# Performance work log

Measured on AMD Instinct MI355X. Metric: run time of the kernel, lower is better.

The kernel has to match this reference:

```python
import jax, jax.numpy as jnp
import numpy as np

GROUP_SIZE = 64

def setup_inputs() -> dict:
    key = jax.random.key(0)
    ks = jax.random.split(key, 7)
    T, N, K, NG = 4096, 4096, 11264, 4096 // GROUP_SIZE
    x = jax.random.normal(ks[0], (T, N), dtype=jnp.float32)
    Q = jax.random.randint(ks[1], (K, N), 0, 8, dtype=jnp.int32)  # uint8 3-bit codes
    scales = jax.random.uniform(ks[2], (K, NG), dtype=jnp.float32)
    zeros = jax.random.uniform(ks[3], (K, NG), dtype=jnp.float32) * 7.0
    mu1 = jax.random.uniform(ks[4], (N,), dtype=jnp.float32) + 0.5
    mu2 = jax.random.uniform(ks[5], (K,), dtype=jnp.float32) + 0.5
    bias = jax.random.normal(ks[6], (K,), dtype=jnp.float32)
    return {"x": x, "Q": Q, "scales": scales, "zeros": zeros, "mu1": mu1, "mu2": mu2, "bias": bias}

def reference(x, Q, scales, zeros, mu1, mu2, bias):
    K, N = Q.shape
    ng = scales.shape[1]
    # group-wise dequant: (Q - zero) * scale, groups along N
    Qg = Q.astype(jnp.float32).reshape(K, ng, GROUP_SIZE)
    W_deq_norm = ((Qg - zeros[:, :, None]) * scales[:, :, None]).reshape(K, N)
    # Sinkhorn mu rescale: per-row mu2, per-column mu1
    W_deq = W_deq_norm * mu2[:, None] * mu1[None, :]
    out = x @ W_deq.T + bias
    return out
```

## Files before the change

kernel.cpp:

```cpp
#include <hip/hip_runtime.h>
#include <stdint.h>
#include <stddef.h>


typedef __attribute__((ext_vector_type(8))) short bfrag;
typedef __attribute__((ext_vector_type(4))) float f32x4;
typedef __attribute__((ext_vector_type(4))) int   i32x4;

__device__ __forceinline__ short f2bf(float f) {
    uint32_t u = __float_as_uint(f);
    u += 0x7fffu + ((u >> 16) & 1u);
    return (short)(u >> 16);
}

__device__ __forceinline__ void gload_lds16(const void* g, void* l) {
    __builtin_amdgcn_global_load_lds(
        (const __attribute__((address_space(1))) void*)g,
        (__attribute__((address_space(3))) void*)l,
        16, 0, 0);
}

__global__ void cvt_x_kernel(const float* __restrict__ x, short* __restrict__ xb) {
    size_t i = (size_t)blockIdx.x * 256 + threadIdx.x;
    const f32x4* xv = (const f32x4*)x + 4 * i;
    f32x4 a = xv[0], b = xv[1], c = xv[2], d = xv[3];
    bfrag o0, o1;
    o0[0] = f2bf(a[0]); o0[1] = f2bf(a[1]); o0[2] = f2bf(a[2]); o0[3] = f2bf(a[3]);
    o0[4] = f2bf(b[0]); o0[5] = f2bf(b[1]); o0[6] = f2bf(b[2]); o0[7] = f2bf(b[3]);
    o1[0] = f2bf(c[0]); o1[1] = f2bf(c[1]); o1[2] = f2bf(c[2]); o1[3] = f2bf(c[3]);
    o1[4] = f2bf(d[0]); o1[5] = f2bf(d[1]); o1[6] = f2bf(d[2]); o1[7] = f2bf(d[3]);
    bfrag* ov = (bfrag*)xb + 2 * i;
    ov[0] = o0; ov[1] = o1;
}

__global__ void deq_w_kernel(const int* __restrict__ Q,
                             const float* __restrict__ scales,
                             const float* __restrict__ zeros,
                             const float* __restrict__ mu1,
                             const float* __restrict__ mu2,
                             short* __restrict__ wb,
                             int k0, int N, int NG) {
    const int kl = blockIdx.x;
    const int kg = k0 + kl;
    const int t  = threadIdx.x;
    const int n0 = t << 4;
    const int g  = n0 >> 6;
    const float s = scales[(size_t)kg * NG + g] * mu2[kg];
    const float z = zeros[(size_t)kg * NG + g];
    const i32x4* qv = (const i32x4*)(Q + (size_t)kg * N + n0);
    const f32x4* uv = (const f32x4*)(mu1 + n0);
    i32x4 q0 = qv[0], q1 = qv[1], q2 = qv[2], q3 = qv[3];
    f32x4 u0 = uv[0], u1 = uv[1], u2 = uv[2], u3 = uv[3];
    bfrag o0, o1;
    o0[0] = f2bf(((float)q0[0] - z) * s * u0[0]);
    o0[1] = f2bf(((float)q0[1] - z) * s * u0[1]);
    o0[2] = f2bf(((float)q0[2] - z) * s * u0[2]);
    o0[3] = f2bf(((float)q0[3] - z) * s * u0[3]);
    o0[4] = f2bf(((float)q1[0] - z) * s * u1[0]);
    o0[5] = f2bf(((float)q1[1] - z) * s * u1[1]);
    o0[6] = f2bf(((float)q1[2] - z) * s * u1[2]);
    o0[7] = f2bf(((float)q1[3] - z) * s * u1[3]);
    o1[0] = f2bf(((float)q2[0] - z) * s * u2[0]);
    o1[1] = f2bf(((float)q2[1] - z) * s * u2[1]);
    o1[2] = f2bf(((float)q2[2] - z) * s * u2[2]);
    o1[3] = f2bf(((float)q2[3] - z) * s * u2[3]);
    o1[4] = f2bf(((float)q3[0] - z) * s * u3[0]);
    o1[5] = f2bf(((float)q3[1] - z) * s * u3[1]);
    o1[6] = f2bf(((float)q3[2] - z) * s * u3[2]);
    o1[7] = f2bf(((float)q3[3] - z) * s * u3[3]);
    bfrag* ov = (bfrag*)(wb + (size_t)kl * N + n0);
    ov[0] = o0; ov[1] = o1;
}


__global__ __launch_bounds__(512, 2)
void gemm8p_kernel(const short* __restrict__ A, const short* __restrict__ B,
                   const float* __restrict__ bias, float* __restrict__ C,
                   int Kc, int Nout, int col0, int GX) {
    extern __shared__ __attribute__((aligned(16))) char smem[];

    const int tid  = threadIdx.x;
    const int lane = tid & 63;
    const int wid  = tid >> 6;
    const int wm   = wid >> 2;
    const int wn   = wid & 3;
    const int r    = lane & 15;
    const int hib  = (lane >> 4) << 4;
    const int sw   = (r & 7) << 4;

    const int nwg = (int)gridDim.x;
    const int cpx = nwg >> 3;
    const int bid = (int)blockIdx.x;
    const int swz = (bid & 7) * cpx + (bid >> 3);
    const int bx  = swz % GX;
    const int by  = swz / GX;
    const int bm  = by * 256;
    const int bnl = bx * 256;

    const int KB = Kc * 2;
    const int swcol = ((tid ^ (tid >> 3)) & 7) << 4;
    const char* srcA = (const char*)A + (size_t)(bm  + (tid >> 3)) * KB + swcol;
    const char* srcB = (const char*)B + (size_t)(bnl + (tid >> 3)) * KB + swcol;

    f32x4 acc[8][4];
#pragma unroll
    for (int i = 0; i < 8; i++)
#pragma unroll
        for (int j = 0; j < 4; j++)
            acc[i][j] = (f32x4){0.f, 0.f, 0.f, 0.f};

    const int NT = Kc / 64;

#define STG_A(t, q) gload_lds16(srcA + (size_t)(t) * 128 + (size_t)(q) * 64 * KB, \
                                smem + ((t) & 1) * 65536 + (q) * 8192 + (tid << 4))
#define STG_B(t, q) gload_lds16(srcB + (size_t)(t) * 128 + (size_t)(q) * 64 * KB, \
                                smem + ((t) & 1) * 65536 + 32768 + (q) * 8192 + (tid << 4))
#define LDF(base, row, s) (*(const bfrag*)((base) + (size_t)(row) * 128 + (((s) * 64 + hib) ^ sw)))
#define MM(I, J, AF, BF) acc[I][J] = __builtin_amdgcn_mfma_f32_16x16x32_bf16(AF, BF, acc[I][J], 0, 0, 0)

#define PH(BUF, MQ, NQ, STAGES, VM) do {                                        \
    const char* Ab_ = smem + (BUF) * 65536;                                     \
    const char* Bb_ = Ab_ + 32768;                                              \
    const int ra_ = wm * 128 + (MQ) * 64 + r;                                   \
    const int rb_ = wn * 64 + (NQ) * 32 + r;                                    \
    bfrag a00_ = LDF(Ab_, ra_,      0), a01_ = LDF(Ab_, ra_,      1);           \
    bfrag a10_ = LDF(Ab_, ra_ + 16, 0), a11_ = LDF(Ab_, ra_ + 16, 1);           \
    bfrag a20_ = LDF(Ab_, ra_ + 32, 0), a21_ = LDF(Ab_, ra_ + 32, 1);           \
    bfrag a30_ = LDF(Ab_, ra_ + 48, 0), a31_ = LDF(Ab_, ra_ + 48, 1);           \
    bfrag b00_ = LDF(Bb_, rb_,      0), b01_ = LDF(Bb_, rb_,      1);           \
    bfrag b10_ = LDF(Bb_, rb_ + 16, 0), b11_ = LDF(Bb_, rb_ + 16, 1);           \
    STAGES;                                                                     \
    __builtin_amdgcn_s_barrier();                                               \
    asm volatile("s_waitcnt lgkmcnt(0)" ::: "memory");                          \
    __builtin_amdgcn_s_setprio(1);                                              \
    MM((MQ)*4 + 0, (NQ)*2 + 0, a00_, b00_); MM((MQ)*4 + 0, (NQ)*2 + 0, a01_, b01_); \
    MM((MQ)*4 + 0, (NQ)*2 + 1, a00_, b10_); MM((MQ)*4 + 0, (NQ)*2 + 1, a01_, b11_); \
    MM((MQ)*4 + 1, (NQ)*2 + 0, a10_, b00_); MM((MQ)*4 + 1, (NQ)*2 + 0, a11_, b01_); \
    MM((MQ)*4 + 1, (NQ)*2 + 1, a10_, b10_); MM((MQ)*4 + 1, (NQ)*2 + 1, a11_, b11_); \
    MM((MQ)*4 + 2, (NQ)*2 + 0, a20_, b00_); MM((MQ)*4 + 2, (NQ)*2 + 0, a21_, b01_); \
    MM((MQ)*4 + 2, (NQ)*2 + 1, a20_, b10_); MM((MQ)*4 + 2, (NQ)*2 + 1, a21_, b11_); \
    MM((MQ)*4 + 3, (NQ)*2 + 0, a30_, b00_); MM((MQ)*4 + 3, (NQ)*2 + 0, a31_, b01_); \
    MM((MQ)*4 + 3, (NQ)*2 + 1, a30_, b10_); MM((MQ)*4 + 3, (NQ)*2 + 1, a31_, b11_); \
    __builtin_amdgcn_s_setprio(0);                                              \
    VM;                                                                         \
    __builtin_amdgcn_s_barrier();                                               \
} while (0)

    STG_A(0, 0); STG_A(0, 1); STG_A(0, 2); STG_A(0, 3);
    STG_B(0, 0); STG_B(0, 1); STG_B(0, 2); STG_B(0, 3);
    STG_A(1, 0); STG_A(1, 2);
    asm volatile("s_waitcnt vmcnt(2)" ::: "memory");
    __builtin_amdgcn_s_barrier();

    for (int it = 0; it < NT / 2; ++it) {
        const int tb = 2 * it + 1;
        int tc = 2 * it + 2; if (tc > NT - 1) tc = NT - 1;
        int td = 2 * it + 3; if (td > NT - 1) td = NT - 1;
        PH(0, 0, 0, { STG_A(tb, 1); STG_A(tb, 3); STG_B(tb, 0); }, (void)0);
        PH(0, 0, 1, { STG_B(tb, 1); STG_B(tb, 2); STG_B(tb, 3); }, (void)0);
        PH(0, 1, 0, { STG_A(tc, 0); STG_A(tc, 2); }, (void)0);
        PH(0, 1, 1, {}, asm volatile("s_waitcnt vmcnt(2)" ::: "memory"));
        PH(1, 0, 0, { STG_A(tc, 1); STG_A(tc, 3); STG_B(tc, 0); }, (void)0);
        PH(1, 0, 1, { STG_B(tc, 1); STG_B(tc, 2); STG_B(tc, 3); }, (void)0);
        PH(1, 1, 0, { STG_A(td, 0); STG_A(td, 2); }, (void)0);
        PH(1, 1, 1, {}, asm volatile("s_waitcnt vmcnt(2)" ::: "memory"));
    }

#undef PH
#undef MM
#undef LDF
#undef STG_A
#undef STG_B

    const int row0 = bm + wm * 128 + (lane >> 4) * 4;
    const int colg = col0 + bnl + wn * 64 + r;
#pragma unroll
    for (int j = 0; j < 4; ++j) {
        const int col = colg + j * 16;
        const float bv = bias[col];
#pragma unroll
        for (int i = 0; i < 8; ++i) {
            const int row = row0 + i * 16;
#pragma unroll
            for (int q = 0; q < 4; ++q)
                C[(size_t)(row + q) * Nout + col] = acc[i][j][q] + bv;
        }
    }
}

__global__ void naive_kernel(const float* __restrict__ x, const int* __restrict__ Q,
                             const float* __restrict__ scales, const float* __restrict__ zeros,
                             const float* __restrict__ mu1, const float* __restrict__ mu2,
                             const float* __restrict__ bias, float* __restrict__ out,
                             int T, int N, int K, int NG) {
    long long total = (long long)T * K;
    for (long long idx = blockIdx.x * 256ll + threadIdx.x; idx < total;
         idx += (long long)gridDim.x * 256ll) {
        int t = (int)(idx / K);
        int k = (int)(idx - (long long)t * K);
        float s = 0.f;
        for (int n = 0; n < N; n++) {
            int g = n >> 6;
            float w = ((float)Q[(size_t)k * N + n] - zeros[(size_t)k * NG + g]) *
                      scales[(size_t)k * NG + g];
            s += x[(size_t)t * N + n] * w * mu1[n];
        }
        out[idx] = s * mu2[k] + bias[k];
    }
}

extern "C" void kernel_launch(void* const* d_in, const int* in_sizes, int n_in,
                              void* d_out, int out_size, void* d_ws, size_t ws_size,
                              hipStream_t stream) {
    const float* x      = (const float*)d_in[0];
    const int*   Q      = (const int*)d_in[1];
    const float* scales = (const float*)d_in[2];
    const float* zeros  = (const float*)d_in[3];
    const float* mu1    = (const float*)d_in[4];
    const float* mu2    = (const float*)d_in[5];
    const float* bias   = (const float*)d_in[6];
    float* out = (float*)d_out;

    const int N  = in_sizes[4];
    const int K  = in_sizes[5];
    const int T  = in_sizes[0] / N;
    const int NG = in_sizes[2] / K;

    const size_t xb_bytes  = (size_t)T * N * 2;
    const size_t row_bytes = (size_t)N * 2;

    const bool shape_ok = (T % 256 == 0) && (K % 256 == 0) &&
                          (N % 128 == 0) && (N % 64 == 0);

    if (!shape_ok || ws_size < xb_bytes + 256 * row_bytes) {
        naive_kernel<<<4096, 256, 0, stream>>>(x, Q, scales, zeros, mu1, mu2,
                                               bias, out, T, N, K, NG);
        return;
    }

    static bool attr_done = false;
    if (!attr_done) {
        (void)hipFuncSetAttribute(reinterpret_cast<const void*>(gemm8p_kernel),
                                  hipFuncAttributeMaxDynamicSharedMemorySize,
                                  131072);
        attr_done = true;
    }

    short* xb = (short*)d_ws;
    short* wb = (short*)((char*)d_ws + xb_bytes);
    size_t max_rows = (ws_size - xb_bytes) / row_bytes;
    int CH = (int)((max_rows / 256) * 256);
    if (CH > K) CH = K;

    cvt_x_kernel<<<(T * N / 16) / 256, 256, 0, stream>>>(x, xb);

    for (int c0 = 0; c0 < K; c0 += CH) {
        int rows = (K - c0 < CH) ? (K - c0) : CH;
        deq_w_kernel<<<rows, 256, 0, stream>>>(Q, scales, zeros, mu1, mu2, wb,
                                               c0, N, NG);
        const int GX = rows / 256;
        dim3 ggrid(GX * (T / 256));
        gemm8p_kernel<<<ggrid, 512, 131072, stream>>>(xb, wb, bias, out,
                                                      N, K, c0, GX);
    }
}
```

Measured before the change: 732.5 us.

## Reuse LDS fragments across GEMM quadrants and use grid-stride prep kernels

The GEMM main loop now keeps the A and B fragments in register arrays and reorders the quadrant visits as 00, 01, 11, 10, so A or B fragments are reused across consecutive quadrants. This cuts LDS reads per K-step (A read twice instead of four times, B read twice per buffer) at the cost of holding more fragment registers live. The x conversion and weight dequant kernels become grid-stride/row-loop kernels that handle 4 elements per thread per step, and the shape check now requires N divisible by 1024. The extra live fragments may raise register pressure at 2 waves per SIMD occupancy.

Result: faster. 684.9 us (-6.5%).

```diff
diff --git a/kernel.cpp b/kernel.cpp
--- a/kernel.cpp
+++ b/kernel.cpp
@@ -4,6 +4,7 @@
 
 
 typedef __attribute__((ext_vector_type(8))) short bfrag;
+typedef __attribute__((ext_vector_type(4))) short s16x4;
 typedef __attribute__((ext_vector_type(4))) float f32x4;
 typedef __attribute__((ext_vector_type(4))) int   i32x4;
 
@@ -20,17 +21,16 @@
         16, 0, 0);
 }
 
-__global__ void cvt_x_kernel(const float* __restrict__ x, short* __restrict__ xb) {
-    size_t i = (size_t)blockIdx.x * 256 + threadIdx.x;
-    const f32x4* xv = (const f32x4*)x + 4 * i;
-    f32x4 a = xv[0], b = xv[1], c = xv[2], d = xv[3];
-    bfrag o0, o1;
-    o0[0] = f2bf(a[0]); o0[1] = f2bf(a[1]); o0[2] = f2bf(a[2]); o0[3] = f2bf(a[3]);
-    o0[4] = f2bf(b[0]); o0[5] = f2bf(b[1]); o0[6] = f2bf(b[2]); o0[7] = f2bf(b[3]);
-    o1[0] = f2bf(c[0]); o1[1] = f2bf(c[1]); o1[2] = f2bf(c[2]); o1[3] = f2bf(c[3]);
-    o1[4] = f2bf(d[0]); o1[5] = f2bf(d[1]); o1[6] = f2bf(d[2]); o1[7] = f2bf(d[3]);
-    bfrag* ov = (bfrag*)xb + 2 * i;
-    ov[0] = o0; ov[1] = o1;
+__global__ void cvt_x_kernel(const float* __restrict__ x, short* __restrict__ xb,
+                             int total4) {
+    for (int i = blockIdx.x * 256 + threadIdx.x; i < total4;
+         i += gridDim.x * 256) {
+        f32x4 a = ((const f32x4*)x)[i];
+        s16x4 o;
+        o[0] = f2bf(a[0]); o[1] = f2bf(a[1]);
+        o[2] = f2bf(a[2]); o[3] = f2bf(a[3]);
+        ((s16x4*)xb)[i] = o;
+    }
 }
 
 __global__ void deq_w_kernel(const int* __restrict__ Q,
@@ -42,34 +42,24 @@
                              int k0, int N, int NG) {
     const int kl = blockIdx.x;
     const int kg = k0 + kl;
-    const int t  = threadIdx.x;
-    const int n0 = t << 4;
-    const int g  = n0 >> 6;
-    const float s = scales[(size_t)kg * NG + g] * mu2[kg];
-    const float z = zeros[(size_t)kg * NG + g];
-    const i32x4* qv = (const i32x4*)(Q + (size_t)kg * N + n0);
-    const f32x4* uv = (const f32x4*)(mu1 + n0);
-    i32x4 q0 = qv[0], q1 = qv[1], q2 = qv[2], q3 = qv[3];
-    f32x4 u0 = uv[0], u1 = uv[1], u2 = uv[2], u3 = uv[3];
-    bfrag o0, o1;
-    o0[0] = f2bf(((float)q0[0] - z) * s * u0[0]);
-    o0[1] = f2bf(((float)q0[1] - z) * s * u0[1]);
-    o0[2] = f2bf(((float)q0[2] - z) * s * u0[2]);
-    o0[3] = f2bf(((float)q0[3] - z) * s * u0[3]);
-    o0[4] = f2bf(((float)q1[0] - z) * s * u1[0]);
-    o0[5] = f2bf(((float)q1[1] - z) * s * u1[1]);
-    o0[6] = f2bf(((float)q1[2] - z) * s * u1[2]);
-    o0[7] = f2bf(((float)q1[3] - z) * s * u1[3]);
-    o1[0] = f2bf(((float)q2[0] - z) * s * u2[0]);
-    o1[1] = f2bf(((float)q2[1] - z) * s * u2[1]);
-    o1[2] = f2bf(((float)q2[2] - z) * s * u2[2]);
-    o1[3] = f2bf(((float)q2[3] - z) * s * u2[3]);
-    o1[4] = f2bf(((float)q3[0] - z) * s * u3[0]);
-    o1[5] = f2bf(((float)q3[1] - z) * s * u3[1]);
-    o1[6] = f2bf(((float)q3[2] - z) * s * u3[2]);
-    o1[7] = f2bf(((float)q3[3] - z) * s * u3[3]);
-    bfrag* ov = (bfrag*)(wb + (size_t)kl * N + n0);
-    ov[0] = o0; ov[1] = o1;
+    const float m2 = mu2[kg];
+    const int*   qrow = Q + (size_t)kg * N;
+    const float* srow = scales + (size_t)kg * NG;
+    const float* zrow = zeros + (size_t)kg * NG;
+    short*       orow = wb + (size_t)kl * N;
+    for (int n0 = threadIdx.x * 4; n0 < N; n0 += 1024) {
+        const int g = n0 >> 6;
+        const float s = srow[g] * m2;
+        const float z = zrow[g];
+        i32x4 q = *(const i32x4*)(qrow + n0);
+        f32x4 u = *(const f32x4*)(mu1 + n0);
+        s16x4 o;
+        o[0] = f2bf(((float)q[0] - z) * s * u[0]);
+        o[1] = f2bf(((float)q[1] - z) * s * u[1]);
+        o[2] = f2bf(((float)q[2] - z) * s * u[2]);
+        o[3] = f2bf(((float)q[3] - z) * s * u[3]);
+        *(s16x4*)(orow + n0) = o;
+    }
 }
 
 
@@ -118,32 +108,29 @@
 #define LDF(base, row, s) (*(const bfrag*)((base) + (size_t)(row) * 128 + (((s) * 64 + hib) ^ sw)))
 #define MM(I, J, AF, BF) acc[I][J] = __builtin_amdgcn_mfma_f32_16x16x32_bf16(AF, BF, acc[I][J], 0, 0, 0)
 
-#define PH(BUF, MQ, NQ, STAGES, VM) do {                                        \
-    const char* Ab_ = smem + (BUF) * 65536;                                     \
-    const char* Bb_ = Ab_ + 32768;                                              \
-    const int ra_ = wm * 128 + (MQ) * 64 + r;                                   \
-    const int rb_ = wn * 64 + (NQ) * 32 + r;                                    \
-    bfrag a00_ = LDF(Ab_, ra_,      0), a01_ = LDF(Ab_, ra_,      1);           \
-    bfrag a10_ = LDF(Ab_, ra_ + 16, 0), a11_ = LDF(Ab_, ra_ + 16, 1);           \
-    bfrag a20_ = LDF(Ab_, ra_ + 32, 0), a21_ = LDF(Ab_, ra_ + 32, 1);           \
-    bfrag a30_ = LDF(Ab_, ra_ + 48, 0), a31_ = LDF(Ab_, ra_ + 48, 1);           \
-    bfrag b00_ = LDF(Bb_, rb_,      0), b01_ = LDF(Bb_, rb_,      1);           \
-    bfrag b10_ = LDF(Bb_, rb_ + 16, 0), b11_ = LDF(Bb_, rb_ + 16, 1);           \
-    STAGES;                                                                     \
+#define RD_A(Ab_, MQ) do { const int ra_ = wm * 128 + (MQ) * 64 + r;            \
+    Af[0] = LDF(Ab_, ra_,      0); Af[1] = LDF(Ab_, ra_,      1);               \
+    Af[2] = LDF(Ab_, ra_ + 16, 0); Af[3] = LDF(Ab_, ra_ + 16, 1);               \
+    Af[4] = LDF(Ab_, ra_ + 32, 0); Af[5] = LDF(Ab_, ra_ + 32, 1);               \
+    Af[6] = LDF(Ab_, ra_ + 48, 0); Af[7] = LDF(Ab_, ra_ + 48, 1); } while (0)
+
+#define RD_B(Bb_, NQ, BF) do { const int rb_ = wn * 64 + (NQ) * 32 + r;         \
+    BF[0] = LDF(Bb_, rb_,      0); BF[1] = LDF(Bb_, rb_,      1);               \
+    BF[2] = LDF(Bb_, rb_ + 16, 0); BF[3] = LDF(Bb_, rb_ + 16, 1); } while (0)
+
+#define QUAD(MQ, NQ, BF) do {                                                   \
     __builtin_amdgcn_s_barrier();                                               \
     asm volatile("s_waitcnt lgkmcnt(0)" ::: "memory");                          \
     __builtin_amdgcn_s_setprio(1);                                              \
-    MM((MQ)*4 + 0, (NQ)*2 + 0, a00_, b00_); MM((MQ)*4 + 0, (NQ)*2 + 0, a01_, b01_); \
-    MM((MQ)*4 + 0, (NQ)*2 + 1, a00_, b10_); MM((MQ)*4 + 0, (NQ)*2 + 1, a01_, b11_); \
-    MM((MQ)*4 + 1, (NQ)*2 + 0, a10_, b00_); MM((MQ)*4 + 1, (NQ)*2 + 0, a11_, b01_); \
-    MM((MQ)*4 + 1, (NQ)*2 + 1, a10_, b10_); MM((MQ)*4 + 1, (NQ)*2 + 1, a11_, b11_); \
-    MM((MQ)*4 + 2, (NQ)*2 + 0, a20_, b00_); MM((MQ)*4 + 2, (NQ)*2 + 0, a21_, b01_); \
-    MM((MQ)*4 + 2, (NQ)*2 + 1, a20_, b10_); MM((MQ)*4 + 2, (NQ)*2 + 1, a21_, b11_); \
-    MM((MQ)*4 + 3, (NQ)*2 + 0, a30_, b00_); MM((MQ)*4 + 3, (NQ)*2 + 0, a31_, b01_); \
-    MM((MQ)*4 + 3, (NQ)*2 + 1, a30_, b10_); MM((MQ)*4 + 3, (NQ)*2 + 1, a31_, b11_); \
+    MM((MQ)*4 + 0, (NQ)*2 + 0, Af[0], BF[0]); MM((MQ)*4 + 0, (NQ)*2 + 0, Af[1], BF[1]); \
+    MM((MQ)*4 + 0, (NQ)*2 + 1, Af[0], BF[2]); MM((MQ)*4 + 0, (NQ)*2 + 1, Af[1], BF[3]); \
+    MM((MQ)*4 + 1, (NQ)*2 + 0, Af[2], BF[0]); MM((MQ)*4 + 1, (NQ)*2 + 0, Af[3], BF[1]); \
+    MM((MQ)*4 + 1, (NQ)*2 + 1, Af[2], BF[2]); MM((MQ)*4 + 1, (NQ)*2 + 1, Af[3], BF[3]); \
+    MM((MQ)*4 + 2, (NQ)*2 + 0, Af[4], BF[0]); MM((MQ)*4 + 2, (NQ)*2 + 0, Af[5], BF[1]); \
+    MM((MQ)*4 + 2, (NQ)*2 + 1, Af[4], BF[2]); MM((MQ)*4 + 2, (NQ)*2 + 1, Af[5], BF[3]); \
+    MM((MQ)*4 + 3, (NQ)*2 + 0, Af[6], BF[0]); MM((MQ)*4 + 3, (NQ)*2 + 0, Af[7], BF[1]); \
+    MM((MQ)*4 + 3, (NQ)*2 + 1, Af[6], BF[2]); MM((MQ)*4 + 3, (NQ)*2 + 1, Af[7], BF[3]); \
     __builtin_amdgcn_s_setprio(0);                                              \
-    VM;                                                                         \
-    __builtin_amdgcn_s_barrier();                                               \
 } while (0)
 
     STG_A(0, 0); STG_A(0, 1); STG_A(0, 2); STG_A(0, 3);
@@ -152,25 +139,63 @@
     asm volatile("s_waitcnt vmcnt(2)" ::: "memory");
     __builtin_amdgcn_s_barrier();
 
+    bfrag Af[8], B0f[4], B1f[4];
+
     for (int it = 0; it < NT / 2; ++it) {
         const int tb = 2 * it + 1;
         int tc = 2 * it + 2; if (tc > NT - 1) tc = NT - 1;
         int td = 2 * it + 3; if (td > NT - 1) td = NT - 1;
-        PH(0, 0, 0, { STG_A(tb, 1); STG_A(tb, 3); STG_B(tb, 0); }, (void)0);
-        PH(0, 0, 1, { STG_B(tb, 1); STG_B(tb, 2); STG_B(tb, 3); }, (void)0);
-        PH(0, 1, 0, { STG_A(tc, 0); STG_A(tc, 2); }, (void)0);
-        PH(0, 1, 1, {}, asm volatile("s_waitcnt vmcnt(2)" ::: "memory"));
-        PH(1, 0, 0, { STG_A(tc, 1); STG_A(tc, 3); STG_B(tc, 0); }, (void)0);
-        PH(1, 0, 1, { STG_B(tc, 1); STG_B(tc, 2); STG_B(tc, 3); }, (void)0);
-        PH(1, 1, 0, { STG_A(td, 0); STG_A(td, 2); }, (void)0);
-        PH(1, 1, 1, {}, asm volatile("s_waitcnt vmcnt(2)" ::: "memory"));
-    }
-
-#undef PH
+        const char* Ab0 = smem;
+        const char* Bb0 = smem + 32768;
+        const char* Ab1 = smem + 65536;
+        const char* Bb1 = smem + 98304;
+
+        RD_A(Ab0, 0); RD_B(Bb0, 0, B0f);
+        STG_A(tb, 1); STG_A(tb, 3); STG_B(tb, 0);
+        QUAD(0, 0, B0f);
+        __builtin_amdgcn_s_barrier();
+
+        RD_B(Bb0, 1, B1f);
+        STG_B(tb, 1); STG_B(tb, 2); STG_B(tb, 3);
+        QUAD(0, 1, B1f);
+        __builtin_amdgcn_s_barrier();
+
+        RD_A(Ab0, 1);
+        STG_A(tc, 0); STG_A(tc, 2);
+        QUAD(1, 1, B1f);
+        __builtin_amdgcn_s_barrier();
+
+        QUAD(1, 0, B0f);
+        asm volatile("s_waitcnt vmcnt(2)" ::: "memory");
+        __builtin_amdgcn_s_barrier();
+
+        RD_A(Ab1, 0); RD_B(Bb1, 0, B0f);
+        STG_A(tc, 1); STG_A(tc, 3); STG_B(tc, 0);
+        QUAD(0, 0, B0f);
+        __builtin_amdgcn_s_barrier();
+
+        RD_B(Bb1, 1, B1f);
+        STG_B(tc, 1); STG_B(tc, 2); STG_B(tc, 3);
+        QUAD(0, 1, B1f);
+        __builtin_amdgcn_s_barrier();
+
+        RD_A(Ab1, 1);
+        STG_A(td, 0); STG_A(td, 2);
+        QUAD(1, 1, B1f);
+        __builtin_amdgcn_s_barrier();
+
+        QUAD(1, 0, B0f);
+        asm volatile("s_waitcnt vmcnt(2)" ::: "memory");
+        __builtin_amdgcn_s_barrier();
+    }
+
+#undef QUAD
+#undef RD_B
+#undef RD_A
 #undef MM
 #undef LDF
+#undef STG_B
 #undef STG_A
-#undef STG_B
 
     const int row0 = bm + wm * 128 + (lane >> 4) * 4;
     const int colg = col0 + bnl + wn * 64 + r;
@@ -230,7 +255,7 @@
     const size_t row_bytes = (size_t)N * 2;
 
     const bool shape_ok = (T % 256 == 0) && (K % 256 == 0) &&
-                          (N % 128 == 0) && (N % 64 == 0);
+                          (N % 1024 == 0) && (N % 128 == 0);
 
     if (!shape_ok || ws_size < xb_bytes + 256 * row_bytes) {
         naive_kernel<<<4096, 256, 0, stream>>>(x, Q, scales, zeros, mu1, mu2,
@@ -252,7 +277,7 @@
     int CH = (int)((max_rows / 256) * 256);
     if (CH > K) CH = K;
 
-    cvt_x_kernel<<<(T * N / 16) / 256, 256, 0, stream>>>(x, xb);
+    cvt_x_kernel<<<2048, 256, 0, stream>>>(x, xb, T * (N / 4));
 
     for (int c0 = 0; c0 < K; c0 += CH) {
         int rows = (K - c0 < CH) ? (K - c0) : CH;
```
